# Optimization experiments

Measured on AMD Instinct MI355X. Metric: run time of the kernel, lower is better.

The kernel has to match this reference:

```python
import jax, jax.numpy as jnp
import numpy as np
from jax import lax

N_POINTS = 4096
D_FEAT = 64


def setup_inputs() -> dict:
    key = jax.random.key(0)
    x = jax.random.normal(key, (N_POINTS, D_FEAT), dtype=jnp.float32)
    return {"x": x}


def _pairwise_dist(x):
    # Euclidean distance matrix [n, n]; diagonal masked to +inf so a point
    # never pairs with itself. Diagonal of D2 is set to 1.0 (not 0) before
    # sqrt so the backward pass is NaN-free.
    sq = jnp.sum(x * x, axis=1)
    D2 = sq[:, None] + sq[None, :] - 2.0 * (x @ x.T)
    n = x.shape[0]
    eye = jnp.eye(n, dtype=bool)
    D2 = jnp.where(eye, 1.0, jnp.maximum(D2, 1e-12))
    D = jnp.sqrt(D2)
    return jnp.where(eye, jnp.inf, D)


def _h0_flag_diagram(D):
    # Dim-0 persistence of the Rips (flag) filtration: every vertex is born at
    # filtration value 0; the n-1 finite deaths are exactly the edge lengths of
    # the minimum spanning tree of the distance graph. Computed with Prim's
    # algorithm vectorized over the frontier (one lax.scan step per MST edge).
    n = D.shape[0]
    intree0 = jnp.zeros((n,), dtype=bool).at[0].set(True)
    mind0 = D[0]  # min distance from the tree to each vertex

    def step(carry, _):
        mind, intree = carry
        masked = jnp.where(intree, jnp.inf, mind)
        j = jnp.argmin(masked)          # next vertex merged into the tree
        death = masked[j]               # edge length at which its class dies
        intree = intree.at[j].set(True)
        mind = jnp.minimum(mind, D[j])
        return (mind, intree), death

    _, deaths = lax.scan(step, (mind0, intree0), None, length=n - 1)
    births = jnp.zeros_like(deaths)
    return jnp.stack([births, deaths], axis=1)  # [n-1, 2]


def reference(x):
    D = _pairwise_dist(x)
    dgm0 = _h0_flag_diagram(D)
    return dgm0
```

## Files before the change

### kernel.cpp

```cpp
#include <hip/hip_runtime.h>
#include <math.h>


#define N 4096
#define DF 64
#define INF __builtin_huge_valf()

__global__ __launch_bounds__(256) void build_d_kernel(const float* __restrict__ x,
                                                      float* __restrict__ D,
                                                      unsigned long long* __restrict__ best) {
    __shared__ float As[64][68];
    __shared__ float Bs[64][68];
    __shared__ float Ts[64][68];
    __shared__ unsigned long long colbuf[64][16];
    const int t = threadIdx.x;

    int br = 0;
    {
        int rem = blockIdx.x;
        while (rem >= 64 - br) {
            rem -= 64 - br;
            ++br;
        }
        br = br;
        int bc = br + rem;
        const int bi = br * 64;
        const int bj = bc * 64;

#pragma unroll
        for (int g = 0; g < 4; ++g) {
            int idx = t + 256 * g;
            int row = idx >> 4;
            int k4 = (idx & 15) << 2;
            *(float4*)(&As[row][k4]) =
                *(const float4*)(x + (size_t)(bi + row) * DF + k4);
            *(float4*)(&Bs[row][k4]) =
                *(const float4*)(x + (size_t)(bj + row) * DF + k4);
        }
        __syncthreads();

        const int ti = (t >> 4) << 2;
        const int tj = (t & 15) << 2;
        float acc[4][4];
#pragma unroll
        for (int r = 0; r < 4; ++r)
#pragma unroll
            for (int c = 0; c < 4; ++c) acc[r][c] = 0.0f;

        for (int k = 0; k < 64; k += 4) {
            float4 a[4], b[4];
#pragma unroll
            for (int r = 0; r < 4; ++r) a[r] = *(const float4*)(&As[ti + r][k]);
#pragma unroll
            for (int c = 0; c < 4; ++c) b[c] = *(const float4*)(&Bs[tj + c][k]);
#pragma unroll
            for (int r = 0; r < 4; ++r)
#pragma unroll
                for (int c = 0; c < 4; ++c) {
                    float d0 = a[r].x - b[c].x;
                    float d1 = a[r].y - b[c].y;
                    float d2 = a[r].z - b[c].z;
                    float d3 = a[r].w - b[c].w;
                    float s = acc[r][c];
                    s = fmaf(d0, d0, s);
                    s = fmaf(d1, d1, s);
                    s = fmaf(d2, d2, s);
                    s = fmaf(d3, d3, s);
                    acc[r][c] = s;
                }
        }

        float val[4][4];
#pragma unroll
        for (int r = 0; r < 4; ++r) {
            int i = bi + ti + r;
            float4 v;
            float* vp = &v.x;
            unsigned long long mk = ~0ULL;
#pragma unroll
            for (int c = 0; c < 4; ++c) {
                int j = bj + tj + c;
                float w = (i == j) ? INF : sqrtf(fmaxf(acc[r][c], 1e-12f));
                val[r][c] = w;
                vp[c] = w;
                unsigned long long key =
                    ((unsigned long long)__float_as_uint(w) << 24) |
                    ((unsigned long long)(unsigned)i << 12) | (unsigned)j;
                mk = key < mk ? key : mk;
            }
            *(float4*)(D + (size_t)i * N + (bj + tj)) = v;
#pragma unroll
            for (int m = 1; m < 16; m <<= 1) {
                unsigned long long o = __shfl_xor(mk, m, 64);
                mk = o < mk ? o : mk;
            }
            if ((t & 15) == 0) atomicMin(&best[i], mk);
        }

        if (br != bc) {
#pragma unroll
            for (int c = 0; c < 4; ++c) {
                unsigned long long ck = ~0ULL;
                int j = bj + tj + c;
#pragma unroll
                for (int r = 0; r < 4; ++r) {
                    int i = bi + ti + r;
                    float w = val[r][c];
                    Ts[tj + c][ti + r] = w;
                    unsigned long long key =
                        ((unsigned long long)__float_as_uint(w) << 24) |
                        ((unsigned long long)(unsigned)j << 12) | (unsigned)i;
                    ck = key < ck ? key : ck;
                }
                colbuf[tj + c][t >> 4] = ck;
            }
            __syncthreads();
            {
                int row = t >> 2;
                int seg = (t & 3) * 16;
                float4* dst = (float4*)(D + (size_t)(bj + row) * N + bi + seg);
#pragma unroll
                for (int q = 0; q < 4; ++q)
                    dst[q] = *(const float4*)(&Ts[row][seg + 4 * q]);
            }
            if (t < 64) {
                unsigned long long k = ~0ULL;
#pragma unroll
                for (int i2 = 0; i2 < 16; ++i2) {
                    unsigned long long v2 = colbuf[t][i2];
                    k = v2 < k ? v2 : k;
                }
                atomicMin(&best[bj + t], k);
            }
        }
    }
}

__global__ __launch_bounds__(256) void init_kernel(unsigned* comp,
                                                   unsigned long long* best,
                                                   unsigned* nedges, unsigned* done) {
    int i = blockIdx.x * 256 + threadIdx.x;
    if (i < N) {
        comp[i] = (unsigned)i;
        best[i] = ~0ULL;
    }
    if (i == 0) { *nedges = 0u; *done = 0u; }
}

__global__ __launch_bounds__(256) void minedge_d_kernel(const float* __restrict__ D,
                                                        const unsigned* __restrict__ comp,
                                                        unsigned long long* __restrict__ best,
                                                        const unsigned* __restrict__ done) {
    if (*done) return;
    __shared__ unsigned compc[N];
    __shared__ unsigned long long keybuf[256];
    const int t = threadIdx.x;
    const int b = blockIdx.x;
    const int r = t >> 4;
    const int j = t & 15;
    const int rowv = b * 16 + r;

    for (int v = t; v < N; v += 256) compc[v] = comp[v];
    __syncthreads();
    const unsigned cr = compc[rowv];
    const float4* rowp = (const float4*)(D + (size_t)rowv * N);
    unsigned long long mykey = ~0ULL;
#pragma unroll 4
    for (int k = 0; k < 64; ++k) {
        float4 v4 = rowp[j + 16 * k];
        int c0 = 4 * (j + 16 * k);
        const float* vp = &v4.x;
#pragma unroll
        for (int q = 0; q < 4; ++q) {
            int c = c0 + q;
            if (compc[c] != cr) {
                unsigned long long key =
                    ((unsigned long long)__float_as_uint(vp[q]) << 24) |
                    ((unsigned long long)(unsigned)rowv << 12) | (unsigned)c;
                mykey = key < mykey ? key : mykey;
            }
        }
    }
    keybuf[t] = mykey;
    __syncthreads();
    if (t < 16) {
        unsigned long long k = ~0ULL;
#pragma unroll
        for (int i = 0; i < 16; ++i) {
            unsigned long long v2 = keybuf[t * 16 + i];
            k = v2 < k ? v2 : k;
        }
        if (k != ~0ULL) atomicMin(&best[compc[b * 16 + t]], k);
    }
}

__global__ __launch_bounds__(256) void minedge_kernel(const float* __restrict__ x,
                                                      const unsigned* __restrict__ comp,
                                                      unsigned long long* __restrict__ best,
                                                      const unsigned* __restrict__ done) {
    if (*done) return;
    __shared__ float xr[16][64];
    __shared__ float xc[64][68];
    __shared__ unsigned compr[16];
    __shared__ unsigned compc[64];
    __shared__ unsigned long long keybuf[256];
    const int t = threadIdx.x;
    const int b = blockIdx.x;
    const int r = t >> 4;
    const int rowv = b * 16 + r;

    {
        int row = t >> 4, f4 = t & 15;
        *(float4*)&xr[row][f4 * 4] =
            *(const float4*)(x + (size_t)(b * 16 + row) * DF + f4 * 4);
        if (t < 16) compr[t] = comp[b * 16 + t];
    }
    __syncthreads();
    const unsigned cr = compr[r];
    unsigned long long mykey = ~0ULL;

    for (int tile = 0; tile < 64; ++tile) {
        {
#pragma unroll
            for (int q = 0; q < 4; ++q) {
                int idx = t + 256 * q;
                int col = idx >> 4, k4 = (idx & 15) * 4;
                *(float4*)&xc[col][k4] =
                    *(const float4*)(x + (size_t)(tile * 64 + col) * DF + k4);
            }
            if (t < 64) compc[t] = comp[tile * 64 + t];
        }
        __syncthreads();
#pragma unroll
        for (int q = 0; q < 4; ++q) {
            int c = (t & 15) + 16 * q;
            unsigned cc = compc[c];
            if (cc != cr) {
                float s = 0.0f;
#pragma unroll
                for (int k = 0; k < 64; k += 4) {
                    float4 a = *(const float4*)&xr[r][k];
                    float4 bb = *(const float4*)&xc[c][k];
                    float d0 = a.x - bb.x;
                    float d1 = a.y - bb.y;
                    float d2 = a.z - bb.z;
                    float d3 = a.w - bb.w;
                    s = fmaf(d0, d0, s);
                    s = fmaf(d1, d1, s);
                    s = fmaf(d2, d2, s);
                    s = fmaf(d3, d3, s);
                }
                float w = sqrtf(fmaxf(s, 1e-12f));
                unsigned long long key =
                    ((unsigned long long)__float_as_uint(w) << 24) |
                    ((unsigned long long)(unsigned)rowv << 12) |
                    (unsigned)(tile * 64 + c);
                mykey = key < mykey ? key : mykey;
            }
        }
        __syncthreads();
    }
    keybuf[t] = mykey;
    __syncthreads();
    if (t < 16) {
        unsigned long long k = ~0ULL;
#pragma unroll
        for (int i = 0; i < 16; ++i) {
            unsigned long long v2 = keybuf[t * 16 + i];
            k = v2 < k ? v2 : k;
        }
        if (k != ~0ULL) atomicMin(&best[compr[t]], k);
    }
}

__global__ void merge_kernel(unsigned* comp, unsigned long long* best,
                             unsigned long long* edges, unsigned* nedges,
                             unsigned* done) {
    if (*done) return;
    __shared__ unsigned cl[N];
    __shared__ unsigned np[N];
    __shared__ unsigned cnt;
    const int t = threadIdx.x;
    const int bs = blockDim.x;
    for (int v = t; v < N; v += bs) cl[v] = comp[v];
    __syncthreads();
    for (int v = t; v < N; v += bs) {
        unsigned p;
        if (cl[v] == (unsigned)v) {
            unsigned long long k = best[v];
            p = (k != ~0ULL) ? cl[(unsigned)(k & 0xFFFu)] : (unsigned)v;
        } else {
            p = cl[v];
        }
        np[v] = p;
    }
    __syncthreads();
    for (int v = t; v < N; v += bs) {
        if (cl[v] == (unsigned)v) {
            unsigned p = np[v];
            if (p != (unsigned)v) {
                bool mutual = (np[p] == (unsigned)v);
                if (mutual && (unsigned)v < p) {
                    np[v] = (unsigned)v;
                } else {
                    unsigned idx = atomicAdd(nedges, 1u);
                    edges[idx] = best[v];
                }
            }
        }
    }
    __syncthreads();
    for (int it = 0; it < 12; ++it) {
        for (int v = t; v < N; v += bs) np[v] = np[np[v]];
        __syncthreads();
    }
    if (t == 0) cnt = 0;
    __syncthreads();
    unsigned local = 0;
    for (int v = t; v < N; v += bs) {
        comp[v] = np[v];
        best[v] = ~0ULL;
        if (np[v] == (unsigned)v) ++local;
    }
    atomicAdd(&cnt, local);
    __syncthreads();
    if (t == 0 && cnt == 1u) *done = 1u;
}

__global__ __launch_bounds__(1024) void replay_kernel(
        const unsigned long long* __restrict__ edges,
        const unsigned* __restrict__ nedges, float* __restrict__ out) {
    __shared__ __align__(16) unsigned char pool[156680];
    __shared__ unsigned chg;
    unsigned* off = (unsigned*)(pool + 65536);
    unsigned long long* ent = (unsigned long long*)(pool + 0);
    unsigned short* par = (unsigned short*)(pool + 81928);
    unsigned* keyw = (unsigned*)(pool + 90120);
    unsigned long long* key64 = (unsigned long long*)(pool + 0);
    unsigned long long* order = (unsigned long long*)(pool + 0);
    unsigned* ptr = (unsigned*)(pool + 106504);
    unsigned short* rankA = (unsigned short*)(pool + 106504);
    unsigned short* nxtA = (unsigned short*)(pool + 122888);
    unsigned short* twin = (unsigned short*)(pool + 139272);
    unsigned* Sa = (unsigned*)(pool + 32768);
    unsigned* Sb = (unsigned*)(pool + 49152);
    unsigned* T = (unsigned*)(pool + 65536);
    unsigned* vA = (unsigned*)(pool + 122888);
    unsigned* jA = (unsigned*)(pool + 139272);
    unsigned* vB = (unsigned*)(pool + 0);
    unsigned* jB = (unsigned*)(pool + 16384);
    unsigned* csum = (unsigned*)(pool + 155656);
    const int t = threadIdx.x;
    const unsigned ne = *nedges;
    const int ns = 2 * (int)ne;

    for (int v = t; v < N; v += 1024) off[v] = 0u;
    if (t == 0) off[N] = 0u;
    for (int k = t; k < N - 1; k += 1024) out[2 * k] = 0.0f;
    __syncthreads();
    for (int e = t; e < (int)ne; e += 1024) {
        unsigned long long k = edges[e];
        atomicAdd(&off[(unsigned)(k >> 12) & 0xFFFu], 1u);
        atomicAdd(&off[(unsigned)k & 0xFFFu], 1u);
    }
    __syncthreads();
    unsigned sloc = 0;
    unsigned loc[16];
    if (t < 256) {
        int base = t * 16;
#pragma unroll
        for (int i = 0; i < 16; ++i) {
            unsigned d = off[base + i];
            loc[i] = sloc;
            sloc += d;
        }
        csum[t] = sloc;
    }
    __syncthreads();
    for (int d = 1; d < 256; d <<= 1) {
        unsigned addv = 0;
        if (t < 256 && t >= d) addv = csum[t - d];
        __syncthreads();
        if (t < 256) csum[t] += addv;
        __syncthreads();
    }
    if (t < 256) {
        int base = t * 16;
        unsigned excl = csum[t] - sloc;
#pragma unroll
        for (int i = 0; i < 16; ++i) {
            unsigned o = loc[i] + excl;
            off[base + i] = o;
            keyw[base + i] = o;
        }
        if (t == 255) off[N] = csum[255];
    }
    __syncthreads();
    for (int e = t; e < (int)ne; e += 1024) {
        unsigned long long k = edges[e];
        unsigned a = (unsigned)(k >> 12) & 0xFFFu;
        unsigned b = (unsigned)k & 0xFFFu;
        unsigned long long wb = k >> 24;
        unsigned p1 = atomicAdd(&keyw[a], 1u);
        unsigned p2 = atomicAdd(&keyw[b], 1u);
        ent[p1] = (wb << 12) | b;
        ent[p2] = (wb << 12) | a;
        twin[p1] = (unsigned short)p2;
        twin[p2] = (unsigned short)p1;
    }
    __syncthreads();
    const unsigned s0 = off[0];
    for (int s = t; s < ns; s += 1024) {
        unsigned v = (unsigned)ent[s] & 0xFFFu;
        unsigned t2 = twin[s];
        unsigned nx = t2 + 1u;
        if (nx == off[v + 1]) nx = off[v];
        if (nx == s0) nx = 0xFFFFu;
        nxtA[s] = (unsigned short)nx;
        rankA[s] = 1;
    }
    __syncthreads();
    for (int round = 0; round < 13; ++round) {
        unsigned short rr[8], nn[8];
#pragma unroll
        for (int q = 0; q < 8; ++q) {
            int s = t + 1024 * q;
            rr[q] = 0;
            nn[q] = 0xFFFFu;
            if (s < ns) {
                unsigned n2 = nxtA[s];
                if (n2 != 0xFFFFu) {
                    rr[q] = rankA[n2];
                    nn[q] = nxtA[n2];
                }
            }
        }
        __syncthreads();
#pragma unroll
        for (int q = 0; q < 8; ++q) {
            int s = t + 1024 * q;
            if (s < ns && nxtA[s] != 0xFFFFu) {
                rankA[s] = (unsigned short)(rankA[s] + rr[q]);
                nxtA[s] = nn[q];
            }
        }
        __syncthreads();
    }
    for (int s = t; s < ns; s += 1024) {
        unsigned t2 = twin[s];
        if (rankA[s] > rankA[t2]) {
            unsigned v = (unsigned)ent[s] & 0xFFFu;
            par[v] = (unsigned short)((unsigned)ent[t2] & 0xFFFu);
            keyw[v] = (unsigned)(ent[s] >> 12);
        }
    }
    if (t == 0) {
        par[0] = 0;
        chg = 0u;
    }
    __syncthreads();
    for (int v = t; v < N; v += 1024) {
        key64[v] = (v == 0) ? ~0ULL
                            : (((unsigned long long)keyw[v]) << 24) |
                                  ((unsigned long long)par[v] << 12) | (unsigned)v;
    }
    __syncthreads();
    for (int v = t; v < N; v += 1024) ptr[v] = (v == 0) ? 0u : (unsigned)par[v];
    __syncthreads();
    for (;;) {
        for (int v = t; v < N; v += 1024) {
            unsigned p = ptr[v];
            if (key64[p] <= key64[v]) {
                unsigned q = ptr[p];
                if (q != p) {
                    ptr[v] = q;
                    chg = 1u;
                }
            }
        }
        __syncthreads();
        unsigned fin = (chg == 0u);
        __syncthreads();
        if (t == 0) chg = 0u;
        __syncthreads();
        if (fin) break;
    }
    unsigned* Sc = Sa;
    unsigned* Sn = Sb;
    for (int v = t; v < N; v += 1024) Sc[v] = 1u;
    __syncthreads();
    for (int round = 0; round < 64; ++round) {
        for (int v = t; v < N; v += 1024) Sn[v] = 1u;
        __syncthreads();
        for (int v = t; v < N; v += 1024)
            if (v != 0) atomicAdd(&Sn[ptr[v]], Sc[v]);
        __syncthreads();
        for (int v = t; v < N; v += 1024)
            if (Sn[v] != Sc[v]) chg = 1u;
        __syncthreads();
        unsigned fin = (chg == 0u);
        __syncthreads();
        if (t == 0) chg = 0u;
        __syncthreads();
        unsigned* tmp = Sc; Sc = Sn; Sn = tmp;
        if (fin) break;
    }
    for (int v = t; v < N; v += 1024) {
        order[v] = (v == 0)
                       ? (0xFFFFFull << 44)
                       : (((unsigned long long)ptr[v]) << 44) |
                             (((unsigned long long)keyw[v]) << 12) | (unsigned)v;
    }
    __syncthreads();
    for (unsigned k = 2; k <= 4096; k <<= 1) {
        for (unsigned j = k >> 1; j >= 4; j >>= 1) {
            for (unsigned i = t; i < 4096; i += 1024) {
                unsigned p = i ^ j;
                if (p > i) {
                    unsigned long long a = order[i], b = order[p];
                    bool up = ((i & k) == 0);
                    if ((a > b) == up) {
                        order[i] = b;
                        order[p] = a;
                    }
                }
            }
            __syncthreads();
        }
        {
            int base = 4 * t;
            unsigned long long e0 = order[base + 0];
            unsigned long long e1 = order[base + 1];
            unsigned long long e2 = order[base + 2];
            unsigned long long e3 = order[base + 3];
            if (k >= 4) {
                bool up = (((unsigned)base & k) == 0);
                unsigned long long tmp;
                if ((e0 > e2) == up) { tmp = e0; e0 = e2; e2 = tmp; }
                if ((e1 > e3) == up) { tmp = e1; e1 = e3; e3 = tmp; }
                if ((e0 > e1) == up) { tmp = e0; e0 = e1; e1 = tmp; }
                if ((e2 > e3) == up) { tmp = e2; e2 = e3; e3 = tmp; }
            } else {
                unsigned long long tmp;
                if (e0 > e1) { tmp = e0; e0 = e1; e1 = tmp; }
                if (e2 < e3) { tmp = e2; e2 = e3; e3 = tmp; }
            }
            order[base + 0] = e0;
            order[base + 1] = e1;
            order[base + 2] = e2;
            order[base + 3] = e3;
            __syncthreads();
        }
    }
    for (int i = t; i < 4096; i += 1024) {
        unsigned vv = (unsigned)order[i] & 0xFFFu;
        T[i] = Sc[vv];
    }
    __syncthreads();
    for (int d = 1; d < 4096; d <<= 1) {
        unsigned addv[4];
#pragma unroll
        for (int q = 0; q < 4; ++q) {
            int i = t + 1024 * q;
            addv[q] = 0;
            if (i >= d && (order[i] >> 44) == (order[i - d] >> 44)) addv[q] = T[i - d];
        }
        __syncthreads();
#pragma unroll
        for (int q = 0; q < 4; ++q) T[t + 1024 * q] += addv[q];
        __syncthreads();
    }
    for (int i = t; i < 4096; i += 1024) {
        unsigned vv = (unsigned)order[i] & 0xFFFu;
        if (vv) {
            vA[vv] = 1u + T[i] - Sc[vv];
            jA[vv] = ptr[vv];
        }
    }
    if (t == 0) {
        vA[0] = 0u;
        jA[0] = 0u;
    }
    __syncthreads();
    {
        unsigned *va = vA, *vb = vB, *ja = jA, *jb = jB;
        for (int r = 0; r < 12; ++r) {
            for (int v = t; v < N; v += 1024) {
                unsigned j2 = ja[v];
                vb[v] = va[v] + va[j2];
                jb[v] = ja[j2];
            }
            __syncthreads();
            unsigned* tmp;
            tmp = va; va = vb; vb = tmp;
            tmp = ja; ja = jb; jb = tmp;
        }
        for (int v = t; v < N; v += 1024) {
            if (v) out[2 * (va[v] - 1) + 1] = __uint_as_float(keyw[v]);
        }
    }
}

extern "C" void kernel_launch(void* const* d_in, const int* in_sizes, int n_in,
                              void* d_out, int out_size, void* d_ws, size_t ws_size,
                              hipStream_t stream) {
    const float* x = (const float*)d_in[0];
    float* out = (float*)d_out;
    const size_t dbytes = (size_t)N * N * 4;

    if (ws_size >= dbytes + 81920) {
        float* D = (float*)d_ws;
        unsigned char* st = (unsigned char*)d_ws + dbytes;
        unsigned long long* best = (unsigned long long*)st;
        unsigned* comp = (unsigned*)(st + 32768);
        unsigned long long* edges = (unsigned long long*)(st + 49152);
        unsigned* nedges = (unsigned*)(st + 81912);
        unsigned* done = (unsigned*)(st + 81916);

        init_kernel<<<16, 256, 0, stream>>>(comp, best, nedges, done);
        build_d_kernel<<<2080, 256, 0, stream>>>(x, D, best);
        merge_kernel<<<1, 1024, 0, stream>>>(comp, best, edges, nedges, done);
        for (int r = 1; r < 12; ++r) {
            minedge_d_kernel<<<256, 256, 0, stream>>>(D, comp, best, done);
            merge_kernel<<<1, 1024, 0, stream>>>(comp, best, edges, nedges, done);
        }
        replay_kernel<<<1, 1024, 0, stream>>>(edges, nedges, out);
    } else {
        unsigned char* ws = (unsigned char*)d_ws;
        unsigned* comp = (unsigned*)ws;
        unsigned long long* best = (unsigned long long*)(ws + 16384);
        unsigned long long* edges = (unsigned long long*)(ws + 49152);
        unsigned* nedges = (unsigned*)(ws + 81920);
        unsigned* done = (unsigned*)(ws + 81984);

        init_kernel<<<16, 256, 0, stream>>>(comp, best, nedges, done);
        for (int r = 0; r < 12; ++r) {
            minedge_kernel<<<256, 256, 0, stream>>>(x, comp, best, done);
            merge_kernel<<<1, 1024, 0, stream>>>(comp, best, edges, nedges, done);
        }
        replay_kernel<<<1, 1024, 0, stream>>>(edges, nedges, out);
    }
}
```

Measured before the change: 472.6 us.

## Fuse Boruvka merge into min-edge kernel with redundant per-block merging

Removes the single-block merge kernel between Boruvka rounds. Every block of the min-edge kernel now recomputes the component merge redundantly in shared memory from the previous round's best keys, and only block 0 writes the edges and the new component array. A triple-buffered best array and double-buffered component arrays avoid races between rounds, and the pointer-jumping loop exits early once nothing changes. This cuts the number of launches and the serial one-block phases, at the cost of repeating merge work in 256 blocks and needing more workspace.

```diff
diff --git a/kernel.cpp b/kernel.cpp
--- a/kernel.cpp
+++ b/kernel.cpp
@@ -22,7 +22,6 @@
             rem -= 64 - br;
             ++br;
         }
-        br = br;
         int bc = br + rem;
         const int bi = br * 64;
         const int bj = bc * 64;
@@ -138,31 +137,110 @@
 
 __global__ __launch_bounds__(256) void init_kernel(unsigned* comp,
                                                    unsigned long long* best,
-                                                   unsigned* nedges, unsigned* done) {
+                                                   unsigned* nedges, unsigned* done,
+                                                   int nbuf) {
     int i = blockIdx.x * 256 + threadIdx.x;
     if (i < N) {
         comp[i] = (unsigned)i;
-        best[i] = ~0ULL;
+        for (int bb = 0; bb < nbuf; ++bb) best[(size_t)bb * N + i] = ~0ULL;
     }
     if (i == 0) { *nedges = 0u; *done = 0u; }
 }
 
-__global__ __launch_bounds__(256) void minedge_d_kernel(const float* __restrict__ D,
-                                                        const unsigned* __restrict__ comp,
-                                                        unsigned long long* __restrict__ best,
-                                                        const unsigned* __restrict__ done) {
+__global__ __launch_bounds__(256) void minedge_lm_kernel(
+        const float* __restrict__ D, const unsigned* __restrict__ compi,
+        unsigned* __restrict__ compo, unsigned long long* __restrict__ best,
+        unsigned long long* edges, unsigned* nedges, unsigned* done, int rnd) {
     if (*done) return;
-    __shared__ unsigned compc[N];
+    __shared__ unsigned cl[N];
+    __shared__ unsigned np[N];
     __shared__ unsigned long long keybuf[256];
+    __shared__ unsigned cnt_sh, chg_sh;
     const int t = threadIdx.x;
     const int b = blockIdx.x;
+    const unsigned long long* bcur = best + (size_t)((rnd - 1) % 3) * N;
+    unsigned long long* bout = best + (size_t)(rnd % 3) * N;
+    unsigned long long* brst = best + (size_t)((rnd + 1) % 3) * N;
+
+    for (int v = t; v < N; v += 256) cl[v] = compi[v];
+    if (t == 0) chg_sh = 0u;
+    __syncthreads();
+
+    unsigned long long kreg[16];
+#pragma unroll
+    for (int i = 0; i < 16; ++i) {
+        int v = t + 256 * i;
+        unsigned p;
+        unsigned long long k = ~0ULL;
+        if (cl[v] == (unsigned)v) {
+            k = bcur[v];
+            p = (k != ~0ULL) ? cl[(unsigned)(k & 0xFFFu)] : (unsigned)v;
+        } else {
+            p = cl[v];
+        }
+        np[v] = p;
+        kreg[i] = k;
+    }
+    __syncthreads();
+#pragma unroll
+    for (int i = 0; i < 16; ++i) {
+        int v = t + 256 * i;
+        if (cl[v] == (unsigned)v) {
+            unsigned p = np[v];
+            if (p != (unsigned)v) {
+                bool mutual = (np[p] == (unsigned)v);
+                if (mutual && (unsigned)v < p) {
+                    np[v] = (unsigned)v;
+                } else if (b == 0) {
+                    unsigned idx = atomicAdd(nedges, 1u);
+                    edges[idx] = kreg[i];
+                }
+            }
+        }
+    }
+    __syncthreads();
+    for (int it = 0; it < 12; ++it) {
+        unsigned any = 0;
+#pragma unroll
+        for (int i = 0; i < 16; ++i) {
+            int v = t + 256 * i;
+            unsigned a = np[v];
+            unsigned g = np[a];
+            if (g != a) {
+                np[v] = g;
+                any = 1u;
+            }
+        }
+        if (any) chg_sh = 1u;
+        __syncthreads();
+        unsigned fin = (chg_sh == 0u);
+        __syncthreads();
+        if (t == 0) chg_sh = 0u;
+        __syncthreads();
+        if (fin) break;
+    }
+    if (t == 0) cnt_sh = 0u;
+    __syncthreads();
+    unsigned local = 0;
+#pragma unroll
+    for (int i = 0; i < 16; ++i) {
+        int v = t + 256 * i;
+        if (np[v] == (unsigned)v) ++local;
+    }
+    atomicAdd(&cnt_sh, local);
+    if (t < 16) brst[b * 16 + t] = ~0ULL;
+    __syncthreads();
+    const bool finished = (cnt_sh == 1u);
+    if (b == 0) {
+        for (int v = t; v < N; v += 256) compo[v] = np[v];
+        if (t == 0 && finished) *done = 1u;
+    }
+    if (finished) return;
+
     const int r = t >> 4;
     const int j = t & 15;
     const int rowv = b * 16 + r;
-
-    for (int v = t; v < N; v += 256) compc[v] = comp[v];
-    __syncthreads();
-    const unsigned cr = compc[rowv];
+    const unsigned cr = np[rowv];
     const float4* rowp = (const float4*)(D + (size_t)rowv * N);
     unsigned long long mykey = ~0ULL;
 #pragma unroll 4
@@ -173,7 +251,7 @@
 #pragma unroll
         for (int q = 0; q < 4; ++q) {
             int c = c0 + q;
-            if (compc[c] != cr) {
+            if (np[c] != cr) {
                 unsigned long long key =
                     ((unsigned long long)__float_as_uint(vp[q]) << 24) |
                     ((unsigned long long)(unsigned)rowv << 12) | (unsigned)c;
@@ -190,7 +268,7 @@
             unsigned long long v2 = keybuf[t * 16 + i];
             k = v2 < k ? v2 : k;
         }
-        if (k != ~0ULL) atomicMin(&best[compc[b * 16 + t]], k);
+        if (k != ~0ULL) atomicMin(&bout[np[b * 16 + t]], k);
     }
 }
 
@@ -273,16 +351,16 @@
     }
 }
 
-__global__ void merge_kernel(unsigned* comp, unsigned long long* best,
-                             unsigned long long* edges, unsigned* nedges,
-                             unsigned* done) {
+__global__ void merge_kernel(const unsigned* compi, unsigned* compo,
+                             unsigned long long* best, unsigned long long* edges,
+                             unsigned* nedges, unsigned* done) {
     if (*done) return;
     __shared__ unsigned cl[N];
     __shared__ unsigned np[N];
     __shared__ unsigned cnt;
     const int t = threadIdx.x;
     const int bs = blockDim.x;
-    for (int v = t; v < N; v += bs) cl[v] = comp[v];
+    for (int v = t; v < N; v += bs) cl[v] = compi[v];
     __syncthreads();
     for (int v = t; v < N; v += bs) {
         unsigned p;
@@ -318,7 +396,7 @@
     __syncthreads();
     unsigned local = 0;
     for (int v = t; v < N; v += bs) {
-        comp[v] = np[v];
+        compo[v] = np[v];
         best[v] = ~0ULL;
         if (np[v] == (unsigned)v) ++local;
     }
@@ -608,22 +686,25 @@
     float* out = (float*)d_out;
     const size_t dbytes = (size_t)N * N * 4;
 
-    if (ws_size >= dbytes + 81920) {
+    if (ws_size >= dbytes + 163840) {
         float* D = (float*)d_ws;
         unsigned char* st = (unsigned char*)d_ws + dbytes;
         unsigned long long* best = (unsigned long long*)st;
-        unsigned* comp = (unsigned*)(st + 32768);
-        unsigned long long* edges = (unsigned long long*)(st + 49152);
-        unsigned* nedges = (unsigned*)(st + 81912);
-        unsigned* done = (unsigned*)(st + 81916);
-
-        init_kernel<<<16, 256, 0, stream>>>(comp, best, nedges, done);
+        unsigned* comp0 = (unsigned*)(st + 98304);
+        unsigned* comp1 = (unsigned*)(st + 114688);
+        unsigned long long* edges = (unsigned long long*)(st + 131072);
+        unsigned* nedges = (unsigned*)(st + 163832);
+        unsigned* done = (unsigned*)(st + 163836);
+
+        init_kernel<<<16, 256, 0, stream>>>(comp0, best, nedges, done, 3);
         build_d_kernel<<<2080, 256, 0, stream>>>(x, D, best);
-        merge_kernel<<<1, 1024, 0, stream>>>(comp, best, edges, nedges, done);
-        for (int r = 1; r < 12; ++r) {
-            minedge_d_kernel<<<256, 256, 0, stream>>>(D, comp, best, done);
-            merge_kernel<<<1, 1024, 0, stream>>>(comp, best, edges, nedges, done);
-        }
+        unsigned* cb[2] = {comp0, comp1};
+        for (int r = 1; r <= 11; ++r) {
+            minedge_lm_kernel<<<256, 256, 0, stream>>>(
+                D, cb[(r - 1) & 1], cb[r & 1], best, edges, nedges, done, r);
+        }
+        merge_kernel<<<1, 1024, 0, stream>>>(cb[1], cb[0], best + (size_t)2 * N,
+                                             edges, nedges, done);
         replay_kernel<<<1, 1024, 0, stream>>>(edges, nedges, out);
     } else {
         unsigned char* ws = (unsigned char*)d_ws;
@@ -633,10 +714,11 @@
         unsigned* nedges = (unsigned*)(ws + 81920);
         unsigned* done = (unsigned*)(ws + 81984);
 
-        init_kernel<<<16, 256, 0, stream>>>(comp, best, nedges, done);
+        init_kernel<<<16, 256, 0, stream>>>(comp, best, nedges, done, 1);
         for (int r = 0; r < 12; ++r) {
             minedge_kernel<<<256, 256, 0, stream>>>(x, comp, best, done);
-            merge_kernel<<<1, 1024, 0, stream>>>(comp, best, edges, nedges, done);
+            merge_kernel<<<1, 1024, 0, stream>>>(comp, comp, best, edges, nedges,
+                                                 done);
         }
         replay_kernel<<<1, 1024, 0, stream>>>(edges, nedges, out);
     }
```

New measurement: 463.5 us. No clear change (-1.9%).
